# Performance work log

Hardware: AMD Instinct MI355X
Metric: run time of the kernel (lower is better)

The kernel has to match this reference:

```python
import jax, jax.numpy as jnp
import numpy as np

N_NODES = 100000
IN_F = 256
OUT_F = 128
N_EDGES = 1600000


def setup_inputs() -> dict:
    key = jax.random.key(0)
    k1, k2, k3, k4 = jax.random.split(key, 4)
    inputs = jax.random.normal(k1, (N_NODES, IN_F), dtype=jnp.float32)
    edge = jax.random.randint(k2, (2, N_EDGES), 0, N_NODES, dtype=jnp.int64)
    # xavier_uniform for weight [in, out]
    bw = float(np.sqrt(6.0 / (IN_F + OUT_F)))
    weight = jax.random.uniform(k3, (IN_F, OUT_F), minval=-bw, maxval=bw, dtype=jnp.float32)
    ba = float(np.sqrt(6.0 / (OUT_F + 1)))
    a = jax.random.uniform(k4, (OUT_F, 1), minval=-ba, maxval=ba, dtype=jnp.float32)
    return {"inputs": inputs, "edge": edge, "weight": weight, "a": a}


def reference(inputs, edge, weight, a):
    # h: [N, out_features]
    h = inputs @ weight
    # edge-wise gather + abs-diff: [E, out_features]
    diff = jnp.abs(h[edge[0]] - h[edge[1]])
    # dot with attention vector a, relu, squeeze -> [E]
    edge_weight = jax.nn.relu((diff @ a).squeeze(-1))
    return (h, edge_weight)
```

## Files before the change

kernel.cpp:

```cpp
#include <hip/hip_runtime.h>
#include <hip/hip_bf16.h>
#include <stdint.h>

typedef __bf16 bf16x8 __attribute__((ext_vector_type(8)));
typedef float  f32x4  __attribute__((ext_vector_type(4)));

#define M_NODES 100000
#define K_IN    256
#define N_OUT   128
#define N_EDGE  1600000

__global__ __launch_bounds__(256) void gemm_h_mfma(
    const float* __restrict__ in,
    const float* __restrict__ w,
    float* __restrict__ h,
    __hip_bfloat16* __restrict__ hmir)
{
    const int lane = threadIdx.x & 63;
    const int wave = threadIdx.x >> 6;
    const int m0   = blockIdx.x * 64;
    const int nb   = wave * 32;

    const int lr = lane & 15;
    const int q  = lane >> 4;

    f32x4 acc[4][2];
    #pragma unroll
    for (int mt = 0; mt < 4; ++mt)
        #pragma unroll
        for (int nt = 0; nt < 2; ++nt)
            acc[mt][nt] = f32x4{0.f, 0.f, 0.f, 0.f};

    for (int kk = 0; kk < K_IN; kk += 32) {
        const int ka = kk + q * 8;

        bf16x8 afrag[4];
        #pragma unroll
        for (int mt = 0; mt < 4; ++mt) {
            const int row = m0 + mt * 16 + lr;
            if (row < M_NODES) {
                const float* ap = in + (size_t)row * K_IN + ka;
                const f32x4 a0 = *(const f32x4*)ap;
                const f32x4 a1 = *(const f32x4*)(ap + 4);
                #pragma unroll
                for (int j = 0; j < 4; ++j) {
                    afrag[mt][j]     = (__bf16)a0[j];
                    afrag[mt][4 + j] = (__bf16)a1[j];
                }
            } else {
                #pragma unroll
                for (int j = 0; j < 8; ++j) afrag[mt][j] = (__bf16)0.f;
            }
        }

        bf16x8 bfrag[2];
        #pragma unroll
        for (int nt = 0; nt < 2; ++nt) {
            const int col = nb + nt * 16 + lr;
            #pragma unroll
            for (int j = 0; j < 8; ++j)
                bfrag[nt][j] = (__bf16)w[(size_t)(ka + j) * N_OUT + col];
        }

        #pragma unroll
        for (int mt = 0; mt < 4; ++mt)
            #pragma unroll
            for (int nt = 0; nt < 2; ++nt)
                acc[mt][nt] = __builtin_amdgcn_mfma_f32_16x16x32_bf16(
                    afrag[mt], bfrag[nt], acc[mt][nt], 0, 0, 0);
    }

    #pragma unroll
    for (int mt = 0; mt < 4; ++mt) {
        const int rb = m0 + mt * 16 + q * 4;
        if (rb >= M_NODES) continue;
        #pragma unroll
        for (int nt = 0; nt < 2; ++nt) {
            const int col = nb + nt * 16 + lr;
            #pragma unroll
            for (int r = 0; r < 4; ++r) {
                const float v = acc[mt][nt][r];
                __builtin_nontemporal_store(v, h + (size_t)(rb + r) * N_OUT + col);
                hmir[(size_t)(rb + r) * N_OUT + col] = __float2bfloat16(v);
            }
        }
    }
}

__device__ inline int detect_i64(const uint32_t* p) {
    return __popcll(__ballot(p[2 * (threadIdx.x & 63) + 1] == 0u)) >= 60;
}

__global__ __launch_bounds__(256) void edge_kernel_bf16(
    const __hip_bfloat16* __restrict__ hm,
    const uint32_t* __restrict__ edge_raw,
    const float* __restrict__ a,
    float* __restrict__ ew,
    int E)
{
    const int e64 = detect_i64(edge_raw);
    const int s = threadIdx.x & 15;
    const int e = (int)((blockIdx.x * 256 + threadIdx.x) >> 4);
    if (e >= E) return;

    int src, dst;
    if (e64) {
        src = (int)edge_raw[2 * (size_t)e];
        dst = (int)edge_raw[2 * ((size_t)E + e)];
    } else {
        const int* e32 = (const int*)edge_raw;
        src = e32[e];
        dst = e32[(size_t)E + e];
    }

    const __bf16* hb = (const __bf16*)hm;
    const bf16x8 hs = *(const bf16x8*)(hb + (size_t)src * N_OUT + s * 8);
    const bf16x8 hd = *(const bf16x8*)(hb + (size_t)dst * N_OUT + s * 8);
    const f32x4 a0 = *(const f32x4*)(a + s * 8);
    const f32x4 a1 = *(const f32x4*)(a + s * 8 + 4);

    float sum = 0.f;
    #pragma unroll
    for (int i = 0; i < 4; ++i)
        sum += fabsf((float)hs[i] - (float)hd[i]) * a0[i];
    #pragma unroll
    for (int i = 0; i < 4; ++i)
        sum += fabsf((float)hs[4 + i] - (float)hd[4 + i]) * a1[i];

    sum += __shfl_xor(sum, 1, 64);
    sum += __shfl_xor(sum, 2, 64);
    sum += __shfl_xor(sum, 4, 64);
    sum += __shfl_xor(sum, 8, 64);

    if (s == 0) ew[e] = fmaxf(sum, 0.f);
}

__global__ __launch_bounds__(256) void edge_kernel_f32(
    const float* __restrict__ h,
    const uint32_t* __restrict__ edge_raw,
    const float* __restrict__ a,
    float* __restrict__ ew,
    int E)
{
    const int e64 = detect_i64(edge_raw);
    const int s = threadIdx.x & 15;
    const int e = (int)((blockIdx.x * 256 + threadIdx.x) >> 4);
    if (e >= E) return;

    int src, dst;
    if (e64) {
        src = (int)edge_raw[2 * (size_t)e];
        dst = (int)edge_raw[2 * ((size_t)E + e)];
    } else {
        const int* e32 = (const int*)edge_raw;
        src = e32[e];
        dst = e32[(size_t)E + e];
    }

    const f32x4 s0 = *(const f32x4*)(h + (size_t)src * N_OUT + s * 8);
    const f32x4 s1 = *(const f32x4*)(h + (size_t)src * N_OUT + s * 8 + 4);
    const f32x4 d0 = *(const f32x4*)(h + (size_t)dst * N_OUT + s * 8);
    const f32x4 d1 = *(const f32x4*)(h + (size_t)dst * N_OUT + s * 8 + 4);
    const f32x4 a0 = *(const f32x4*)(a + s * 8);
    const f32x4 a1 = *(const f32x4*)(a + s * 8 + 4);

    float sum = 0.f;
    #pragma unroll
    for (int i = 0; i < 4; ++i) sum += fabsf(s0[i] - d0[i]) * a0[i];
    #pragma unroll
    for (int i = 0; i < 4; ++i) sum += fabsf(s1[i] - d1[i]) * a1[i];

    sum += __shfl_xor(sum, 1, 64);
    sum += __shfl_xor(sum, 2, 64);
    sum += __shfl_xor(sum, 4, 64);
    sum += __shfl_xor(sum, 8, 64);

    if (s == 0) ew[e] = fmaxf(sum, 0.f);
}

extern "C" void kernel_launch(void* const* d_in, const int* in_sizes, int n_in,
                              void* d_out, int out_size, void* d_ws, size_t ws_size,
                              hipStream_t stream) {
    const float*    in   = (const float*)d_in[0];
    const uint32_t* edge = (const uint32_t*)d_in[1];
    const float*    w    = (const float*)d_in[2];
    const float*    a    = (const float*)d_in[3];

    float* h  = (float*)d_out;
    float* ew = h + (size_t)M_NODES * N_OUT;

    const size_t mirror_bytes = (size_t)M_NODES * N_OUT * sizeof(__hip_bfloat16);
    __hip_bfloat16* hmir =
        (ws_size >= mirror_bytes) ? (__hip_bfloat16*)d_ws : nullptr;

    if (hmir) {
        gemm_h_mfma<<<dim3((M_NODES + 63) / 64), dim3(256), 0, stream>>>(
            in, w, h, hmir);
        const int eblocks = (N_EDGE * 16 + 255) / 256;
        edge_kernel_bf16<<<dim3(eblocks), dim3(256), 0, stream>>>(
            hmir, edge, a, ew, N_EDGE);
    } else {
        gemm_h_mfma<<<dim3((M_NODES + 63) / 64), dim3(256), 0, stream>>>(
            in, w, h, (__hip_bfloat16*)d_ws);
        const int eblocks = (N_EDGE * 16 + 255) / 256;
        edge_kernel_f32<<<dim3(eblocks), dim3(256), 0, stream>>>(
            h, edge, a, ew, N_EDGE);
    }
}
```

Baseline: 324.4 us.

## Pre-transpose weight to bf16 and give each wave full output width

A small prep kernel converts the weight matrix to bf16 and stores it transposed, so GEMM B fragments become single 16-byte loads instead of eight strided scalar float loads with per-element conversion. The GEMM is restructured so each wave owns 16 rows and all 128 output columns. This way every input row is read once per wave instead of being re-read by four waves. It adds an extra kernel launch and workspace space, and raises per-wave B traffic, which should mostly hit cache because the transposed weight is small.

Result: slower. 338.7 us (+4.4%).

```diff
diff --git a/kernel.cpp b/kernel.cpp
--- a/kernel.cpp
+++ b/kernel.cpp
@@ -10,17 +10,84 @@
 #define N_OUT   128
 #define N_EDGE  1600000
 
-__global__ __launch_bounds__(256) void gemm_h_mfma(
+__global__ __launch_bounds__(256) void prep_bt(const float* __restrict__ w,
+                                               __hip_bfloat16* __restrict__ bt) {
+    const int col = blockIdx.x;
+    const int k   = threadIdx.x;
+    bt[(size_t)col * K_IN + k] = __float2bfloat16(w[(size_t)k * N_OUT + col]);
+}
+
+__global__ __launch_bounds__(256) void gemm_h_mfma2(
     const float* __restrict__ in,
-    const float* __restrict__ w,
+    const __hip_bfloat16* __restrict__ bt,
     float* __restrict__ h,
     __hip_bfloat16* __restrict__ hmir)
+{
+    const int lane = threadIdx.x & 63;
+    const int wave = threadIdx.x >> 6;
+    const int lr   = lane & 15;
+    const int q    = lane >> 4;
+    const int m0   = blockIdx.x * 64 + wave * 16;
+    const int row  = m0 + lr;
+    const __bf16* btb = (const __bf16*)bt;
+
+    f32x4 acc[8];
+    #pragma unroll
+    for (int nt = 0; nt < 8; ++nt) acc[nt] = f32x4{0.f, 0.f, 0.f, 0.f};
+
+    for (int kk = 0; kk < K_IN; kk += 32) {
+        const int ka = kk + q * 8;
+
+        bf16x8 afrag;
+        if (row < M_NODES) {
+            const float* ap = in + (size_t)row * K_IN + ka;
+            const f32x4 a0 = *(const f32x4*)ap;
+            const f32x4 a1 = *(const f32x4*)(ap + 4);
+            #pragma unroll
+            for (int j = 0; j < 4; ++j) {
+                afrag[j]     = (__bf16)a0[j];
+                afrag[4 + j] = (__bf16)a1[j];
+            }
+        } else {
+            #pragma unroll
+            for (int j = 0; j < 8; ++j) afrag[j] = (__bf16)0.f;
+        }
+
+        bf16x8 bfrag[8];
+        #pragma unroll
+        for (int nt = 0; nt < 8; ++nt)
+            bfrag[nt] = *(const bf16x8*)(btb + (size_t)(nt * 16 + lr) * K_IN + ka);
+
+        #pragma unroll
+        for (int nt = 0; nt < 8; ++nt)
+            acc[nt] = __builtin_amdgcn_mfma_f32_16x16x32_bf16(
+                afrag, bfrag[nt], acc[nt], 0, 0, 0);
+    }
+
+    const int rb = m0 + q * 4;
+    if (rb < M_NODES) {
+        #pragma unroll
+        for (int nt = 0; nt < 8; ++nt) {
+            const int col = nt * 16 + lr;
+            #pragma unroll
+            for (int r = 0; r < 4; ++r) {
+                const float v = acc[nt][r];
+                __builtin_nontemporal_store(v, h + (size_t)(rb + r) * N_OUT + col);
+                if (hmir)
+                    hmir[(size_t)(rb + r) * N_OUT + col] = __float2bfloat16(v);
+            }
+        }
+    }
+}
+
+__global__ __launch_bounds__(256) void gemm_h_mfma(
+    const float* __restrict__ in, const float* __restrict__ w,
+    float* __restrict__ h, __hip_bfloat16* __restrict__ hmir)
 {
     const int lane = threadIdx.x & 63;
     const int wave = threadIdx.x >> 6;
     const int m0   = blockIdx.x * 64;
     const int nb   = wave * 32;
-
     const int lr = lane & 15;
     const int q  = lane >> 4;
 
@@ -33,7 +100,6 @@
 
     for (int kk = 0; kk < K_IN; kk += 32) {
         const int ka = kk + q * 8;
-
         bf16x8 afrag[4];
         #pragma unroll
         for (int mt = 0; mt < 4; ++mt) {
@@ -44,7 +110,7 @@
                 const f32x4 a1 = *(const f32x4*)(ap + 4);
                 #pragma unroll
                 for (int j = 0; j < 4; ++j) {
-                    afrag[mt][j]     = (__bf16)a0[j];
+                    afrag[mt][j] = (__bf16)a0[j];
                     afrag[mt][4 + j] = (__bf16)a1[j];
                 }
             } else {
@@ -52,7 +118,6 @@
                 for (int j = 0; j < 8; ++j) afrag[mt][j] = (__bf16)0.f;
             }
         }
-
         bf16x8 bfrag[2];
         #pragma unroll
         for (int nt = 0; nt < 2; ++nt) {
@@ -61,7 +126,6 @@
             for (int j = 0; j < 8; ++j)
                 bfrag[nt][j] = (__bf16)w[(size_t)(ka + j) * N_OUT + col];
         }
-
         #pragma unroll
         for (int mt = 0; mt < 4; ++mt)
             #pragma unroll
@@ -69,7 +133,6 @@
                 acc[mt][nt] = __builtin_amdgcn_mfma_f32_16x16x32_bf16(
                     afrag[mt], bfrag[nt], acc[mt][nt], 0, 0, 0);
     }
-
     #pragma unroll
     for (int mt = 0; mt < 4; ++mt) {
         const int rb = m0 + mt * 16 + q * 4;
@@ -81,7 +144,8 @@
             for (int r = 0; r < 4; ++r) {
                 const float v = acc[mt][nt][r];
                 __builtin_nontemporal_store(v, h + (size_t)(rb + r) * N_OUT + col);
-                hmir[(size_t)(rb + r) * N_OUT + col] = __float2bfloat16(v);
+                if (hmir)
+                    hmir[(size_t)(rb + r) * N_OUT + col] = __float2bfloat16(v);
             }
         }
     }
@@ -190,20 +254,27 @@
     float* ew = h + (size_t)M_NODES * N_OUT;
 
     const size_t mirror_bytes = (size_t)M_NODES * N_OUT * sizeof(__hip_bfloat16);
-    __hip_bfloat16* hmir =
-        (ws_size >= mirror_bytes) ? (__hip_bfloat16*)d_ws : nullptr;
-
-    if (hmir) {
-        gemm_h_mfma<<<dim3((M_NODES + 63) / 64), dim3(256), 0, stream>>>(
-            in, w, h, hmir);
-        const int eblocks = (N_EDGE * 16 + 255) / 256;
+    const size_t bt_off   = (mirror_bytes + 255) & ~(size_t)255;
+    const size_t bt_bytes = (size_t)N_OUT * K_IN * sizeof(__hip_bfloat16);
+    const int gblocks = (M_NODES + 63) / 64;
+    const int eblocks = (N_EDGE * 16 + 255) / 256;
+
+    if (ws_size >= bt_off + bt_bytes) {
+        __hip_bfloat16* hmir = (__hip_bfloat16*)d_ws;
+        __hip_bfloat16* bt   = (__hip_bfloat16*)((char*)d_ws + bt_off);
+        prep_bt<<<dim3(N_OUT), dim3(K_IN), 0, stream>>>(w, bt);
+        gemm_h_mfma2<<<dim3(gblocks), dim3(256), 0, stream>>>(in, bt, h, hmir);
         edge_kernel_bf16<<<dim3(eblocks), dim3(256), 0, stream>>>(
             hmir, edge, a, ew, N_EDGE);
-    } else {
-        gemm_h_mfma<<<dim3((M_NODES + 63) / 64), dim3(256), 0, stream>>>(
-            in, w, h, (__hip_bfloat16*)d_ws);
-        const int eblocks = (N_EDGE * 16 + 255) / 256;
+    } else if (ws_size >= bt_bytes) {
+        __hip_bfloat16* bt = (__hip_bfloat16*)d_ws;
+        prep_bt<<<dim3(N_OUT), dim3(K_IN), 0, stream>>>(w, bt);
+        gemm_h_mfma2<<<dim3(gblocks), dim3(256), 0, stream>>>(in, bt, h, nullptr);
         edge_kernel_f32<<<dim3(eblocks), dim3(256), 0, stream>>>(
             h, edge, a, ew, N_EDGE);
-    }
-}
+    } else {
+        gemm_h_mfma<<<dim3(gblocks), dim3(256), 0, stream>>>(in, w, h, nullptr);
+        edge_kernel_f32<<<dim3(eblocks), dim3(256), 0, stream>>>(
+            h, edge, a, ew, N_EDGE);
+    }
+}
```
